# Performance work log

Measured on AMD Instinct MI355X. Metric: run time of the kernel, lower is better.

Reference implementation:

```python
import jax, jax.numpy as jnp
import numpy as np

B, S, H = 2, 1024, 2048          # batch, seq, hidden
E, K = 8, 2                       # num experts, top-k
I = 1408                          # moe_intermediate_size
IS = 5632                         # shared_expert_intermediate_size
WSCALE = 0.02


def setup_inputs() -> dict:
    key = jax.random.key(0)
    ks = jax.random.split(key, 9)
    f32 = jnp.float32
    return {
        "hidden_states": jax.random.normal(ks[0], (B, S, H), dtype=f32),
        "gate_w": jax.random.normal(ks[1], (E, H), dtype=f32) * WSCALE,          # router
        "w_gate": jax.random.normal(ks[2], (E, H, I), dtype=f32) * WSCALE,       # experts.N.gate_proj
        "w_up": jax.random.normal(ks[3], (E, H, I), dtype=f32) * WSCALE,         # experts.N.up_proj
        "w_down": jax.random.normal(ks[4], (E, I, H), dtype=f32) * WSCALE,       # experts.N.down_proj
        "sw_gate": jax.random.normal(ks[5], (H, IS), dtype=f32) * WSCALE,        # shared_expert.gate_proj
        "sw_up": jax.random.normal(ks[6], (H, IS), dtype=f32) * WSCALE,          # shared_expert.up_proj
        "sw_down": jax.random.normal(ks[7], (IS, H), dtype=f32) * WSCALE,        # shared_expert.down_proj
        "shared_gate_w": jax.random.normal(ks[8], (H, 1), dtype=f32) * WSCALE,   # shared_expert_gate
    }


def reference(hidden_states, gate_w, w_gate, w_up, w_down, sw_gate, sw_up, sw_down, shared_gate_w):
    x = hidden_states                                   # [B,S,H]
    # ---- TopKGate: softmax router -> top-k weights + indices, renormalized ----
    logits = jnp.einsum("bsh,eh->bse", x, gate_w)       # [B,S,E]
    probs = jax.nn.softmax(logits, axis=-1)
    top_w, top_i = jax.lax.top_k(probs, K)              # [B,S,K]
    top_w = top_w / jnp.sum(top_w, axis=-1, keepdims=True)
    # dense combine weights per expert: sum_k top_w * (top_i == e)  -> [B,S,E]
    onehot = jax.nn.one_hot(top_i, E, dtype=x.dtype)    # [B,S,K,E]
    combine = jnp.einsum("bsk,bske->bse", top_w, onehot)
    # ---- dense all-experts SwiGLU MLP, then mask/combine (faithful to source) ----
    g = jnp.einsum("bsh,ehi->besi", x, w_gate)          # [B,E,S,I]
    u = jnp.einsum("bsh,ehi->besi", x, w_up)
    h = jax.nn.silu(g) * u
    expert_out = jnp.einsum("besi,eih->besh", h, w_down)  # [B,E,S,H]
    moe_out = jnp.einsum("besh,bse->bsh", expert_out, combine)
    # ---- shared expert with sigmoid gate ----
    sh = jax.nn.silu(x @ sw_gate) * (x @ sw_up)         # [B,S,IS]
    shared_out = sh @ sw_down                            # [B,S,H]
    shared_gate = jax.nn.sigmoid(x @ shared_gate_w)     # [B,S,1]
    return moe_out + shared_out * shared_gate
```

## Files before the change

### kernel.cpp

```cpp
#include <hip/hip_runtime.h>
#include <hip/hip_bf16.h>
#include <stdint.h>

#define TOK   2048
#define HDIM  2048
#define IDIM  1408
#define ISDIM 5632
#define NEXP  8

typedef float  f32x4  __attribute__((ext_vector_type(4)));
typedef short  bf16x8 __attribute__((ext_vector_type(8)));

__device__ __forceinline__ unsigned short f2b(float f) {
  union { float f; uint32_t u; } v; v.f = f;
  return (unsigned short)((v.u + 0x7fffu + ((v.u >> 16) & 1u)) >> 16);
}

__device__ __forceinline__ void async16(void* lds, const void* g) {
  __builtin_amdgcn_global_load_lds(
      (const __attribute__((address_space(1))) unsigned int*)g,
      (__attribute__((address_space(3))) unsigned int*)lds, 16, 0, 0);
}

__global__ __launch_bounds__(256) void router_kernel(
    const float* __restrict__ X, const float* __restrict__ GW,
    const float* __restrict__ SGW, int* __restrict__ cnt,
    int* __restrict__ tok_e, float* __restrict__ tok_w, float* __restrict__ sg)
{
  const int tkn = blockIdx.x, t = threadIdx.x;
  const float* xr = X + (size_t)tkn * HDIM;
  float a[NEXP + 1];
  #pragma unroll
  for (int e = 0; e <= NEXP; ++e) a[e] = 0.f;
  for (int h = t; h < HDIM; h += 256) {
    const float xv = xr[h];
    #pragma unroll
    for (int e = 0; e < NEXP; ++e) a[e] += xv * GW[e * HDIM + h];
    a[NEXP] += xv * SGW[h];
  }
  #pragma unroll
  for (int off = 32; off > 0; off >>= 1) {
    #pragma unroll
    for (int e = 0; e <= NEXP; ++e) a[e] += __shfl_down(a[e], off);
  }
  __shared__ float red[4][NEXP + 1];
  if ((t & 63) == 0) {
    #pragma unroll
    for (int e = 0; e <= NEXP; ++e) red[t >> 6][e] = a[e];
  }
  __syncthreads();
  if (t == 0) {
    float l[NEXP + 1];
    #pragma unroll
    for (int e = 0; e <= NEXP; ++e) l[e] = red[0][e] + red[1][e] + red[2][e] + red[3][e];
    int i1 = 0;
    #pragma unroll
    for (int e = 1; e < NEXP; ++e) if (l[e] > l[i1]) i1 = e;
    int i2 = (i1 == 0) ? 1 : 0;
    #pragma unroll
    for (int e = 0; e < NEXP; ++e) if (e != i1 && e != i2 && l[e] > l[i2]) i2 = e;
    const float w1 = 1.f / (1.f + __expf(l[i2] - l[i1]));
    tok_e[tkn * 2 + 0] = i1; tok_e[tkn * 2 + 1] = i2;
    tok_w[tkn * 2 + 0] = w1; tok_w[tkn * 2 + 1] = 1.f - w1;
    atomicAdd(&cnt[i1], 1); atomicAdd(&cnt[i2], 1);
    sg[tkn] = 1.f / (1.f + __expf(-l[NEXP]));
  }
}

__global__ void scan_kernel(const int* __restrict__ cnt, int* __restrict__ offs) {
  if (threadIdx.x == 0) {
    int r = 0;
    for (int e = 0; e < NEXP; ++e) { offs[e] = r; r += cnt[e]; }
  }
}

__global__ __launch_bounds__(256) void build_kernel(
    const int* __restrict__ tok_e, const float* __restrict__ tok_w,
    const int* __restrict__ offs, int* __restrict__ cur,
    int* __restrict__ list, float* __restrict__ wl)
{
  const int tkn = blockIdx.x * 256 + threadIdx.x;
  if (tkn >= TOK) return;
  #pragma unroll
  for (int k = 0; k < 2; ++k) {
    const int e = tok_e[tkn * 2 + k];
    const int pos = atomicAdd(&cur[e], 1);
    const int slot = offs[e] + pos;
    list[slot] = tkn;
    wl[slot] = tok_w[tkn * 2 + k];
  }
}

__global__ __launch_bounds__(256) void cvt_kernel(
    const float* __restrict__ src, unsigned short* __restrict__ dst, int n4)
{
  const int i = blockIdx.x * 512 + threadIdx.x;
  #pragma unroll
  for (int p = 0; p < 2; ++p) {
    const int j = i + p * 256;
    if (j < n4) {
      const float4 v = ((const float4*)src)[j];
      ushort4 b; b.x = f2b(v.x); b.y = f2b(v.y); b.z = f2b(v.z); b.w = f2b(v.w);
      ((ushort4*)dst)[j] = b;
    }
  }
}

__global__ __launch_bounds__(256) void transpose_cvt_kernel(
    const float* __restrict__ src, unsigned short* __restrict__ dst,
    const int R, const int C)
{
  __shared__ unsigned short tile[64][72];
  const size_t mat = (size_t)blockIdx.z * R * C;
  const int c0 = blockIdx.x * 64, r0 = blockIdx.y * 64;
  const int t = threadIdx.x;
  const int rr = t >> 4, cc = (t & 15) * 4;
  #pragma unroll
  for (int p = 0; p < 4; ++p) {
    const int r = rr + p * 16;
    const float4 v = *(const float4*)(src + mat + (size_t)(r0 + r) * C + c0 + cc);
    tile[cc + 0][r] = f2b(v.x);
    tile[cc + 1][r] = f2b(v.y);
    tile[cc + 2][r] = f2b(v.z);
    tile[cc + 3][r] = f2b(v.w);
  }
  __syncthreads();
  #pragma unroll
  for (int p = 0; p < 2; ++p) {
    const int id = p * 256 + t;
    const int c = id >> 3, q = id & 7;
    const uint4 v = *(const uint4*)&tile[c][q * 8];
    *(uint4*)(dst + mat + (size_t)(c0 + c) * R + r0 + q * 8) = v;
  }
}


template<bool GATHER>
__global__ __launch_bounds__(256) void gateup_bf_kernel(
    const unsigned short* __restrict__ Xb,
    const unsigned short* __restrict__ WgT,
    const unsigned short* __restrict__ WuT,
    unsigned short* __restrict__ Cout,
    const int* __restrict__ list, const int* __restrict__ offs,
    const int* __restrict__ cnt, const int N, const int NT)
{
  __shared__ char smem[49152];
  char* sA  = smem;
  char* sBg = smem + 16384;
  char* sBu = smem + 32768;

  int wg = blockIdx.x;
  wg = (wg & 7) * (gridDim.x >> 3) + (wg >> 3);
  const int mt = wg & 15;
  const int pn = wg >> 4;

  const int t = threadIdx.x;
  int rowbase, mcnt, n0;
  const unsigned short *Wg, *Wu;
  if (GATHER) {
    const int e = pn / NT, n = pn % NT;
    mcnt = cnt[e] - mt * 128;
    if (mcnt <= 0) return;
    rowbase = offs[e] + mt * 128;
    n0 = n * 128;
    Wg = WgT + (size_t)e * N * HDIM;
    Wu = WuT + (size_t)e * N * HDIM;
  } else {
    rowbase = mt * 128;
    mcnt = 128;
    n0 = pn * 128;
    Wg = WgT; Wu = WuT;
  }

  const int w = t >> 6, lane = t & 63;
  const int wr = w >> 1, wc = w & 1;
  const int lcol = lane & 15, lk = lane >> 4;

  f32x4 accg[4][4], accu[4][4];
  #pragma unroll
  for (int i = 0; i < 4; ++i)
    #pragma unroll
    for (int j = 0; j < 4; ++j) { accg[i][j] = {0.f,0.f,0.f,0.f}; accu[i][j] = {0.f,0.f,0.f,0.f}; }

  int arow[4], bm[4], koff[4];
  #pragma unroll
  for (int p = 0; p < 4; ++p) {
    const int s = p * 256 + t;
    const int m = s >> 3;
    bm[p] = m;
    koff[p] = ((s & 7) ^ (m & 7)) << 3;
    arow[p] = GATHER ? list[rowbase + m] : (rowbase + m);
  }

  const int KSTEPS = HDIM / 64;
  for (int kt = 0; kt < KSTEPS; ++kt) {
    const int k0 = kt * 64;
    if (kt) __syncthreads();
    #pragma unroll
    for (int p = 0; p < 4; ++p) {
      const int lb = (p * 256 + (t & 192)) * 16;
      async16(sA  + lb, Xb + (size_t)arow[p] * HDIM + k0 + koff[p]);
      async16(sBg + lb, Wg + (size_t)(n0 + bm[p]) * HDIM + k0 + koff[p]);
      async16(sBu + lb, Wu + (size_t)(n0 + bm[p]) * HDIM + k0 + koff[p]);
    }
    __syncthreads();
    #pragma unroll
    for (int ks = 0; ks < 2; ++ks) {
      bf16x8 af[4], bg[4], bu[4];
      #pragma unroll
      for (int fm = 0; fm < 4; ++fm) {
        const int m = wr * 64 + fm * 16 + lcol;
        af[fm] = *(const bf16x8*)(sA + m * 128 + (((ks * 4 + lk) ^ (m & 7)) << 4));
      }
      #pragma unroll
      for (int fn = 0; fn < 4; ++fn) {
        const int n = wc * 64 + fn * 16 + lcol;
        const int ra = n * 128 + (((ks * 4 + lk) ^ (n & 7)) << 4);
        bg[fn] = *(const bf16x8*)(sBg + ra);
        bu[fn] = *(const bf16x8*)(sBu + ra);
      }
      #pragma unroll
      for (int fm = 0; fm < 4; ++fm)
        #pragma unroll
        for (int fn = 0; fn < 4; ++fn) {
          accg[fm][fn] = __builtin_amdgcn_mfma_f32_16x16x32_bf16(af[fm], bg[fn], accg[fm][fn], 0, 0, 0);
          accu[fm][fn] = __builtin_amdgcn_mfma_f32_16x16x32_bf16(af[fm], bu[fn], accu[fm][fn], 0, 0, 0);
        }
    }
  }
  #pragma unroll
  for (int fm = 0; fm < 4; ++fm) {
    #pragma unroll
    for (int fn = 0; fn < 4; ++fn) {
      const int col = n0 + wc * 64 + fn * 16 + lcol;
      #pragma unroll
      for (int r = 0; r < 4; ++r) {
        const int lrow = wr * 64 + fm * 16 + lk * 4 + r;
        if (lrow < mcnt) {
          const float gv = accg[fm][fn][r];
          const float uv = accu[fm][fn][r];
          const float hv = gv * uv / (1.f + __expf(-gv));
          Cout[(size_t)(rowbase + lrow) * N + col] = f2b(hv);
        }
      }
    }
  }
}

template<bool EXPERT, int KSPLIT>
__global__ __launch_bounds__(256) void down_bf_kernel(
    const unsigned short* __restrict__ Abuf,
    const unsigned short* __restrict__ BT,
    float* __restrict__ out,
    const int* __restrict__ list, const float* __restrict__ wl,
    const int* __restrict__ offs, const int* __restrict__ cnt,
    const int K, const int ktps)
{
  __shared__ char smem[32768];
  char* sA = smem;
  char* sB = smem + 16384;

  int wg = blockIdx.x;
  wg = (wg & 7) * (gridDim.x >> 3) + (wg >> 3);
  const int ksp = wg % KSPLIT;
  const int mt  = (wg / KSPLIT) & 15;
  const int pn  = wg / (KSPLIT * 16);

  const int t = threadIdx.x;
  int rowbase, mcnt, n0;
  const unsigned short* Bm;
  if (EXPERT) {
    const int e = pn >> 4, n = pn & 15;
    mcnt = cnt[e] - mt * 128;
    if (mcnt <= 0) return;
    rowbase = offs[e] + mt * 128;
    n0 = n * 128;
    Bm = BT + (size_t)e * HDIM * K;
  } else {
    rowbase = mt * 128;
    mcnt = 128;
    n0 = pn * 128;
    Bm = BT;
  }
  const int w = t >> 6, lane = t & 63;
  const int wr = w >> 1, wc = w & 1;
  const int lcol = lane & 15, lk = lane >> 4;

  f32x4 acc[4][4];
  #pragma unroll
  for (int i = 0; i < 4; ++i)
    #pragma unroll
    for (int j = 0; j < 4; ++j) acc[i][j] = {0.f,0.f,0.f,0.f};

  int bm[4], koff[4];
  #pragma unroll
  for (int p = 0; p < 4; ++p) {
    const int s = p * 256 + t;
    const int m = s >> 3;
    bm[p] = m;
    koff[p] = ((s & 7) ^ (m & 7)) << 3;
  }

  const int kbeg = ksp * ktps, kend = kbeg + ktps;
  for (int kt = kbeg; kt < kend; ++kt) {
    const int k0 = kt * 64;
    if (kt != kbeg) __syncthreads();
    #pragma unroll
    for (int p = 0; p < 4; ++p) {
      const int lb = (p * 256 + (t & 192)) * 16;
      async16(sA + lb, Abuf + (size_t)(rowbase + bm[p]) * K + k0 + koff[p]);
      async16(sB + lb, Bm + (size_t)(n0 + bm[p]) * K + k0 + koff[p]);
    }
    __syncthreads();
    #pragma unroll
    for (int ks = 0; ks < 2; ++ks) {
      bf16x8 af[4], bfr[4];
      #pragma unroll
      for (int fm = 0; fm < 4; ++fm) {
        const int m = wr * 64 + fm * 16 + lcol;
        af[fm] = *(const bf16x8*)(sA + m * 128 + (((ks * 4 + lk) ^ (m & 7)) << 4));
      }
      #pragma unroll
      for (int fn = 0; fn < 4; ++fn) {
        const int n = wc * 64 + fn * 16 + lcol;
        bfr[fn] = *(const bf16x8*)(sB + n * 128 + (((ks * 4 + lk) ^ (n & 7)) << 4));
      }
      #pragma unroll
      for (int fm = 0; fm < 4; ++fm)
        #pragma unroll
        for (int fn = 0; fn < 4; ++fn)
          acc[fm][fn] = __builtin_amdgcn_mfma_f32_16x16x32_bf16(af[fm], bfr[fn], acc[fm][fn], 0, 0, 0);
    }
  }
  #pragma unroll
  for (int fm = 0; fm < 4; ++fm) {
    #pragma unroll
    for (int fn = 0; fn < 4; ++fn) {
      const int col = n0 + wc * 64 + fn * 16 + lcol;
      #pragma unroll
      for (int r = 0; r < 4; ++r) {
        const int lrow = wr * 64 + fm * 16 + lk * 4 + r;
        if (lrow < mcnt) {
          const float v = acc[fm][fn][r];
          if (EXPERT) {
            const int slot = rowbase + lrow;
            atomicAdd(out + (size_t)list[slot] * HDIM + col, wl[slot] * v);
          } else {
            const int row = rowbase + lrow;
            atomicAdd(out + (size_t)row * HDIM + col, wl[row] * v);
          }
        }
      }
    }
  }
}

template<bool GATHER>
__global__ __launch_bounds__(256) void gateup_kernel(
    const float* __restrict__ X,
    const float* __restrict__ WgA, const float* __restrict__ WuA,
    unsigned short* __restrict__ Cout,
    const int* __restrict__ list, const int* __restrict__ offs,
    const int* __restrict__ cnt, const int N)
{
  __shared__ char smem[49152];
  char* sA  = smem;
  char* sBg = smem + 16384;
  char* sBu = smem + 32768;
  const int t = threadIdx.x;
  const int nt = blockIdx.x;
  int rowbase, mcnt;
  const float *Wg, *Wu;
  if (GATHER) {
    const int e  = blockIdx.y >> 4;
    const int mt = blockIdx.y & 15;
    mcnt = cnt[e] - mt * 128;
    if (mcnt <= 0) return;
    rowbase = offs[e] + mt * 128;
    Wg = WgA + (size_t)e * HDIM * N;
    Wu = WuA + (size_t)e * HDIM * N;
  } else {
    rowbase = blockIdx.y * 128;
    mcnt = 128;
    Wg = WgA; Wu = WuA;
  }
  const int n0 = nt * 128;
  const int w = t >> 6, lane = t & 63;
  const int wr = w >> 1, wc = w & 1;
  const int lcol = lane & 15, lk = lane >> 4;
  f32x4 accg[4][4], accu[4][4];
  #pragma unroll
  for (int i = 0; i < 4; ++i)
    #pragma unroll
    for (int j = 0; j < 4; ++j) { accg[i][j] = {0.f,0.f,0.f,0.f}; accu[i][j] = {0.f,0.f,0.f,0.f}; }
  int arow[8];
  #pragma unroll
  for (int p = 0; p < 8; ++p) {
    const int m = p * 16 + (t >> 4);
    arow[p] = GATHER ? list[rowbase + m] : (rowbase + m);
  }
  const int ak4 = (t & 15) << 2;
  const int bn = t & 127, bkh = t >> 7;
  const int KSTEPS = HDIM / 64;
  for (int kt = 0; kt < KSTEPS; ++kt) {
    const int k0 = kt * 64;
    if (kt) __syncthreads();
    #pragma unroll
    for (int p = 0; p < 8; ++p) {
      const int m = p * 16 + (t >> 4);
      const float4 v = *(const float4*)(X + (size_t)arow[p] * HDIM + k0 + ak4);
      ushort4 b; b.x = f2b(v.x); b.y = f2b(v.y); b.z = f2b(v.z); b.w = f2b(v.w);
      *(ushort4*)(sA + m * 128 + ((((ak4 >> 3) ^ (m & 7)) << 4) | ((ak4 & 7) << 1))) = b;
    }
    #pragma unroll
    for (int p = 0; p < 8; ++p) {
      const int k4 = (p << 1) | bkh;
      const size_t gb = (size_t)(k0 + (k4 << 2)) * N + n0 + bn;
      const int wa = bn * 128 + ((((k4 >> 1) ^ (bn & 7)) << 4) | ((k4 & 1) << 3));
      ushort4 vg, vu;
      vg.x = f2b(Wg[gb]);                 vu.x = f2b(Wu[gb]);
      vg.y = f2b(Wg[gb + (size_t)N]);     vu.y = f2b(Wu[gb + (size_t)N]);
      vg.z = f2b(Wg[gb + 2*(size_t)N]);   vu.z = f2b(Wu[gb + 2*(size_t)N]);
      vg.w = f2b(Wg[gb + 3*(size_t)N]);   vu.w = f2b(Wu[gb + 3*(size_t)N]);
      *(ushort4*)(sBg + wa) = vg;
      *(ushort4*)(sBu + wa) = vu;
    }
    __syncthreads();
    #pragma unroll
    for (int ks = 0; ks < 2; ++ks) {
      bf16x8 af[4], bg[4], bu[4];
      #pragma unroll
      for (int fm = 0; fm < 4; ++fm) {
        const int m = wr * 64 + fm * 16 + lcol;
        af[fm] = *(const bf16x8*)(sA + m * 128 + (((ks * 4 + lk) ^ (m & 7)) << 4));
      }
      #pragma unroll
      for (int fn = 0; fn < 4; ++fn) {
        const int n = wc * 64 + fn * 16 + lcol;
        const int ra = n * 128 + (((ks * 4 + lk) ^ (n & 7)) << 4);
        bg[fn] = *(const bf16x8*)(sBg + ra);
        bu[fn] = *(const bf16x8*)(sBu + ra);
      }
      #pragma unroll
      for (int fm = 0; fm < 4; ++fm)
        #pragma unroll
        for (int fn = 0; fn < 4; ++fn) {
          accg[fm][fn] = __builtin_amdgcn_mfma_f32_16x16x32_bf16(af[fm], bg[fn], accg[fm][fn], 0, 0, 0);
          accu[fm][fn] = __builtin_amdgcn_mfma_f32_16x16x32_bf16(af[fm], bu[fn], accu[fm][fn], 0, 0, 0);
        }
    }
  }
  #pragma unroll
  for (int fm = 0; fm < 4; ++fm) {
    #pragma unroll
    for (int fn = 0; fn < 4; ++fn) {
      const int col = n0 + wc * 64 + fn * 16 + lcol;
      #pragma unroll
      for (int r = 0; r < 4; ++r) {
        const int lrow = wr * 64 + fm * 16 + lk * 4 + r;
        if (lrow < mcnt) {
          const float gv = accg[fm][fn][r];
          const float uv = accu[fm][fn][r];
          Cout[(size_t)(rowbase + lrow) * N + col] = f2b(gv * uv / (1.f + __expf(-gv)));
        }
      }
    }
  }
}

template<bool EXPERT>
__global__ __launch_bounds__(256) void down_kernel(
    const unsigned short* __restrict__ Abuf,
    const float* __restrict__ Ball,
    float* __restrict__ out,
    const int* __restrict__ list, const float* __restrict__ wl,
    const int* __restrict__ offs, const int* __restrict__ cnt, const int K)
{
  __shared__ char smem[32768];
  char* sA = smem;
  char* sB = smem + 16384;
  const int t = threadIdx.x;
  const int nt = blockIdx.x;
  int rowbase, mcnt;
  const float* Bm;
  if (EXPERT) {
    const int e  = blockIdx.y >> 4;
    const int mt = blockIdx.y & 15;
    mcnt = cnt[e] - mt * 128;
    if (mcnt <= 0) return;
    rowbase = offs[e] + mt * 128;
    Bm = Ball + (size_t)e * K * HDIM;
  } else {
    rowbase = blockIdx.y * 128;
    mcnt = 128;
    Bm = Ball;
  }
  const int n0 = nt * 128;
  const int w = t >> 6, lane = t & 63;
  const int wr = w >> 1, wc = w & 1;
  const int lcol = lane & 15, lk = lane >> 4;
  f32x4 acc[4][4];
  #pragma unroll
  for (int i = 0; i < 4; ++i)
    #pragma unroll
    for (int j = 0; j < 4; ++j) acc[i][j] = {0.f,0.f,0.f,0.f};
  const int bn = t & 127, bkh = t >> 7;
  const int KSTEPS = K / 64;
  for (int kt = 0; kt < KSTEPS; ++kt) {
    const int k0 = kt * 64;
    if (kt) __syncthreads();
    #pragma unroll
    for (int p = 0; p < 4; ++p) {
      const int s = p * 256 + t;
      const int m = s >> 3;
      const int k8 = (s & 7) ^ (m & 7);
      const uint4 v = *(const uint4*)(Abuf + (size_t)(rowbase + m) * K + k0 + (k8 << 3));
      *(uint4*)(sA + s * 16) = v;
    }
    #pragma unroll
    for (int p = 0; p < 8; ++p) {
      const int k4 = (p << 1) | bkh;
      const size_t gb = (size_t)(k0 + (k4 << 2)) * HDIM + n0 + bn;
      const int wa = bn * 128 + ((((k4 >> 1) ^ (bn & 7)) << 4) | ((k4 & 1) << 3));
      ushort4 vb;
      vb.x = f2b(Bm[gb]);
      vb.y = f2b(Bm[gb + HDIM]);
      vb.z = f2b(Bm[gb + 2 * HDIM]);
      vb.w = f2b(Bm[gb + 3 * HDIM]);
      *(ushort4*)(sB + wa) = vb;
    }
    __syncthreads();
    #pragma unroll
    for (int ks = 0; ks < 2; ++ks) {
      bf16x8 af[4], bfr[4];
      #pragma unroll
      for (int fm = 0; fm < 4; ++fm) {
        const int m = wr * 64 + fm * 16 + lcol;
        af[fm] = *(const bf16x8*)(sA + m * 128 + (((ks * 4 + lk) ^ (m & 7)) << 4));
      }
      #pragma unroll
      for (int fn = 0; fn < 4; ++fn) {
        const int n = wc * 64 + fn * 16 + lcol;
        bfr[fn] = *(const bf16x8*)(sB + n * 128 + (((ks * 4 + lk) ^ (n & 7)) << 4));
      }
      #pragma unroll
      for (int fm = 0; fm < 4; ++fm)
        #pragma unroll
        for (int fn = 0; fn < 4; ++fn)
          acc[fm][fn] = __builtin_amdgcn_mfma_f32_16x16x32_bf16(af[fm], bfr[fn], acc[fm][fn], 0, 0, 0);
    }
  }
  #pragma unroll
  for (int fm = 0; fm < 4; ++fm) {
    #pragma unroll
    for (int fn = 0; fn < 4; ++fn) {
      const int col = n0 + wc * 64 + fn * 16 + lcol;
      #pragma unroll
      for (int r = 0; r < 4; ++r) {
        const int lrow = wr * 64 + fm * 16 + lk * 4 + r;
        if (lrow < mcnt) {
          const float v = acc[fm][fn][r];
          if (EXPERT) {
            const int slot = rowbase + lrow;
            atomicAdd(out + (size_t)list[slot] * HDIM + col, wl[slot] * v);
          } else {
            const int row = rowbase + lrow;
            out[(size_t)row * HDIM + col] = wl[row] * v;
          }
        }
      }
    }
  }
}

extern "C" void kernel_launch(void* const* d_in, const int* in_sizes, int n_in,
                              void* d_out, int out_size, void* d_ws, size_t ws_size,
                              hipStream_t stream)
{
  const float* x       = (const float*)d_in[0];
  const float* gate_w  = (const float*)d_in[1];
  const float* w_gate  = (const float*)d_in[2];
  const float* w_up    = (const float*)d_in[3];
  const float* w_down  = (const float*)d_in[4];
  const float* sw_gate = (const float*)d_in[5];
  const float* sw_up   = (const float*)d_in[6];
  const float* sw_down = (const float*)d_in[7];
  const float* sgw     = (const float*)d_in[8];

  float* out = (float*)d_out;
  char* ws = (char*)d_ws;

  const size_t NEED = 136000000;

  if (ws_size >= NEED) {
    unsigned short* Xb   = (unsigned short*)ws;
    unsigned short* R1a  = (unsigned short*)(ws + 8388608);
    unsigned short* R1b  = (unsigned short*)(ws + 54525952);
    unsigned short* shb  = (unsigned short*)(ws + 100663296);
    unsigned short* hb   = (unsigned short*)(ws + 123731968);
    char* meta = ws + 135626752;
    int*   cnt   = (int*)(meta);
    int*   cur   = (int*)(meta + 256);
    int*   offs  = (int*)(meta + 512);
    int*   list  = (int*)(meta + 768);
    float* wl    = (float*)(meta + 768 + 17152);
    int*   tok_e = (int*)(meta + 768 + 2 * 17152);
    float* tok_w = (float*)(meta + 768 + 2 * 17152 + 16384);
    float* sg    = (float*)(meta + 768 + 2 * 17152 + 32768);

    hipMemsetAsync(meta, 0, 768 + 2 * 17152, stream);
    hipMemsetAsync(out, 0, (size_t)TOK * HDIM * 4, stream);

    cvt_kernel<<<TOK * HDIM / 4 / 512, 256, 0, stream>>>(x, Xb, TOK * HDIM / 4);
    router_kernel<<<TOK, 256, 0, stream>>>(x, gate_w, sgw, cnt, tok_e, tok_w, sg);
    scan_kernel<<<1, 64, 0, stream>>>(cnt, offs);
    build_kernel<<<8, 256, 0, stream>>>(tok_e, tok_w, offs, cur, list, wl);

    transpose_cvt_kernel<<<dim3(ISDIM / 64, HDIM / 64, 1), 256, 0, stream>>>(sw_gate, R1a, HDIM, ISDIM);
    transpose_cvt_kernel<<<dim3(ISDIM / 64, HDIM / 64, 1), 256, 0, stream>>>(sw_up,   R1b, HDIM, ISDIM);
    gateup_bf_kernel<false><<<704, 256, 0, stream>>>(
        Xb, R1a, R1b, shb, nullptr, nullptr, nullptr, ISDIM, 44);
    transpose_cvt_kernel<<<dim3(HDIM / 64, ISDIM / 64, 1), 256, 0, stream>>>(sw_down, R1a, ISDIM, HDIM);
    down_bf_kernel<false, 2><<<512, 256, 0, stream>>>(
        shb, R1a, out, nullptr, sg, nullptr, nullptr, ISDIM, (ISDIM / 64) / 2);
    transpose_cvt_kernel<<<dim3(IDIM / 64, HDIM / 64, NEXP), 256, 0, stream>>>(w_gate, R1a, HDIM, IDIM);
    transpose_cvt_kernel<<<dim3(IDIM / 64, HDIM / 64, NEXP), 256, 0, stream>>>(w_up,   R1b, HDIM, IDIM);
    gateup_bf_kernel<true><<<1408, 256, 0, stream>>>(
        Xb, R1a, R1b, hb, list, offs, cnt, IDIM, 11);
    transpose_cvt_kernel<<<dim3(HDIM / 64, IDIM / 64, NEXP), 256, 0, stream>>>(w_down, R1a, IDIM, HDIM);
    down_bf_kernel<true, 1><<<2048, 256, 0, stream>>>(
        hb, R1a, out, list, wl, offs, cnt, IDIM, IDIM / 64);
  } else {
    unsigned short* sh_buf = (unsigned short*)ws;
    unsigned short* h_buf  = (unsigned short*)(ws + 23068672);
    char* meta = ws + 34963456;
    int*   cnt   = (int*)(meta);
    int*   cur   = (int*)(meta + 256);
    int*   offs  = (int*)(meta + 512);
    int*   list  = (int*)(meta + 768);
    float* wl    = (float*)(meta + 768 + 17152);
    int*   tok_e = (int*)(meta + 768 + 2 * 17152);
    float* tok_w = (float*)(meta + 768 + 2 * 17152 + 16384);
    float* sg    = (float*)(meta + 768 + 2 * 17152 + 32768);

    hipMemsetAsync(meta, 0, 768 + 2 * 17152, stream);
    router_kernel<<<TOK, 256, 0, stream>>>(x, gate_w, sgw, cnt, tok_e, tok_w, sg);
    scan_kernel<<<1, 64, 0, stream>>>(cnt, offs);
    build_kernel<<<8, 256, 0, stream>>>(tok_e, tok_w, offs, cur, list, wl);
    gateup_kernel<false><<<dim3(ISDIM / 128, TOK / 128), 256, 0, stream>>>(
        x, sw_gate, sw_up, sh_buf, nullptr, nullptr, nullptr, ISDIM);
    down_kernel<false><<<dim3(HDIM / 128, TOK / 128), 256, 0, stream>>>(
        sh_buf, sw_down, out, nullptr, sg, nullptr, nullptr, ISDIM);
    gateup_kernel<true><<<dim3(IDIM / 128, NEXP * 16), 256, 0, stream>>>(
        x, w_gate, w_up, h_buf, list, offs, cnt, IDIM);
    down_kernel<true><<<dim3(HDIM / 128, NEXP * 16), 256, 0, stream>>>(
        h_buf, w_down, out, list, wl, offs, cnt, IDIM);
  }
}
```

Measured before the change: 674.9 us.

## Merge shared and routed expert GEMMs into single gate-up and down launches

Adds a gate-up kernel and a down-projection kernel that each cover both the shared expert and the routed experts in one grid. Block IDs are split by range so that shared and expert tiles run concurrently. This removes the separate launches and the partially filled last waves between the shared and expert phases. It needs a larger workspace so all transposed bf16 weights can be held at once. It also drops the old block-order swizzle and the fp32 fallback path, so a small workspace now leaves no valid code path.

```diff
diff --git a/kernel.cpp b/kernel.cpp
--- a/kernel.cpp
+++ b/kernel.cpp
@@ -134,26 +134,232 @@
   }
 }
 
-
-template<bool GATHER>
-__global__ __launch_bounds__(256) void gateup_bf_kernel(
+__global__ __launch_bounds__(256) void gateup_fused_kernel(
     const unsigned short* __restrict__ Xb,
-    const unsigned short* __restrict__ WgT,
-    const unsigned short* __restrict__ WuT,
-    unsigned short* __restrict__ Cout,
-    const int* __restrict__ list, const int* __restrict__ offs,
-    const int* __restrict__ cnt, const int N, const int NT)
+    const unsigned short* __restrict__ Wshg, const unsigned short* __restrict__ Wshu,
+    const unsigned short* __restrict__ Wexg, const unsigned short* __restrict__ Wexu,
+    unsigned short* __restrict__ shb, unsigned short* __restrict__ hb,
+    const int* __restrict__ list, const int* __restrict__ offs, const int* __restrict__ cnt)
 {
   __shared__ char smem[49152];
   char* sA  = smem;
   char* sBg = smem + 16384;
   char* sBu = smem + 32768;
 
+  const int wg = blockIdx.x;
+  const int mt = wg / 132;
+  const int pn = wg % 132;
+  const int t = threadIdx.x;
+
+  int rowbase, mcnt, n0, N, gather;
+  const unsigned short *Wg, *Wu;
+  unsigned short* Cout;
+  if (pn < 44) {
+    N = ISDIM; n0 = pn * 128; rowbase = mt * 128; mcnt = 128; gather = 0;
+    Wg = Wshg; Wu = Wshu; Cout = shb;
+  } else {
+    const int pnE = pn - 44;
+    const int e = pnE / 11, n = pnE % 11;
+    mcnt = cnt[e] - mt * 128;
+    if (mcnt <= 0) return;
+    N = IDIM; n0 = n * 128; rowbase = offs[e] + mt * 128; gather = 1;
+    Wg = Wexg + (size_t)e * IDIM * HDIM;
+    Wu = Wexu + (size_t)e * IDIM * HDIM;
+    Cout = hb;
+  }
+
+  const int w = t >> 6, lane = t & 63;
+  const int wr = w >> 1, wc = w & 1;
+  const int lcol = lane & 15, lk = lane >> 4;
+
+  f32x4 accg[4][4], accu[4][4];
+  #pragma unroll
+  for (int i = 0; i < 4; ++i)
+    #pragma unroll
+    for (int j = 0; j < 4; ++j) { accg[i][j] = {0.f,0.f,0.f,0.f}; accu[i][j] = {0.f,0.f,0.f,0.f}; }
+
+  int arow[4], bm[4], koff[4];
+  #pragma unroll
+  for (int p = 0; p < 4; ++p) {
+    const int s = p * 256 + t;
+    const int m = s >> 3;
+    bm[p] = m;
+    koff[p] = ((s & 7) ^ (m & 7)) << 3;
+    arow[p] = gather ? list[rowbase + m] : (rowbase + m);
+  }
+
+  const int KSTEPS = HDIM / 64;
+  for (int kt = 0; kt < KSTEPS; ++kt) {
+    const int k0 = kt * 64;
+    if (kt) __syncthreads();
+    #pragma unroll
+    for (int p = 0; p < 4; ++p) {
+      const int lb = (p * 256 + (t & 192)) * 16;
+      async16(sA  + lb, Xb + (size_t)arow[p] * HDIM + k0 + koff[p]);
+      async16(sBg + lb, Wg + (size_t)(n0 + bm[p]) * HDIM + k0 + koff[p]);
+      async16(sBu + lb, Wu + (size_t)(n0 + bm[p]) * HDIM + k0 + koff[p]);
+    }
+    __syncthreads();
+    #pragma unroll
+    for (int ks = 0; ks < 2; ++ks) {
+      bf16x8 af[4], bg[4], bu[4];
+      #pragma unroll
+      for (int fm = 0; fm < 4; ++fm) {
+        const int m = wr * 64 + fm * 16 + lcol;
+        af[fm] = *(const bf16x8*)(sA + m * 128 + (((ks * 4 + lk) ^ (m & 7)) << 4));
+      }
+      #pragma unroll
+      for (int fn = 0; fn < 4; ++fn) {
+        const int n = wc * 64 + fn * 16 + lcol;
+        const int ra = n * 128 + (((ks * 4 + lk) ^ (n & 7)) << 4);
+        bg[fn] = *(const bf16x8*)(sBg + ra);
+        bu[fn] = *(const bf16x8*)(sBu + ra);
+      }
+      #pragma unroll
+      for (int fm = 0; fm < 4; ++fm)
+        #pragma unroll
+        for (int fn = 0; fn < 4; ++fn) {
+          accg[fm][fn] = __builtin_amdgcn_mfma_f32_16x16x32_bf16(af[fm], bg[fn], accg[fm][fn], 0, 0, 0);
+          accu[fm][fn] = __builtin_amdgcn_mfma_f32_16x16x32_bf16(af[fm], bu[fn], accu[fm][fn], 0, 0, 0);
+        }
+    }
+  }
+  #pragma unroll
+  for (int fm = 0; fm < 4; ++fm) {
+    #pragma unroll
+    for (int fn = 0; fn < 4; ++fn) {
+      const int col = n0 + wc * 64 + fn * 16 + lcol;
+      #pragma unroll
+      for (int r = 0; r < 4; ++r) {
+        const int lrow = wr * 64 + fm * 16 + lk * 4 + r;
+        if (lrow < mcnt) {
+          const float gv = accg[fm][fn][r];
+          const float uv = accu[fm][fn][r];
+          const float hv = gv * uv / (1.f + __expf(-gv));
+          Cout[(size_t)(rowbase + lrow) * N + col] = f2b(hv);
+        }
+      }
+    }
+  }
+}
+
+__global__ __launch_bounds__(256) void down_fused_kernel(
+    const unsigned short* __restrict__ shb, const unsigned short* __restrict__ hb,
+    const unsigned short* __restrict__ WdshT, const unsigned short* __restrict__ WdexT,
+    float* __restrict__ out,
+    const int* __restrict__ list, const float* __restrict__ wl, const float* __restrict__ sg,
+    const int* __restrict__ offs, const int* __restrict__ cnt)
+{
+  __shared__ char smem[32768];
+  char* sA = smem;
+  char* sB = smem + 16384;
+
+  const int wg = blockIdx.x;
+  const int t = threadIdx.x;
+  int rowbase, mcnt, n0, K, kbeg, em;
+  const unsigned short *Ap, *Bp;
+  if (wg < 1024) {
+    const int pn = wg & 15, layer = wg >> 4;
+    const int ksp = layer & 3, mt = layer >> 2;
+    rowbase = mt * 128; mcnt = 128; n0 = pn * 128;
+    K = ISDIM; kbeg = ksp * 22; em = 0;
+    Ap = shb; Bp = WdshT;
+  } else {
+    const int wgE = wg - 1024;
+    const int pnE = wgE & 127, mt = wgE >> 7;
+    const int e = pnE >> 4;
+    mcnt = cnt[e] - mt * 128;
+    if (mcnt <= 0) return;
+    rowbase = offs[e] + mt * 128; n0 = (pnE & 15) * 128;
+    K = IDIM; kbeg = 0; em = 1;
+    Ap = hb; Bp = WdexT + (size_t)e * HDIM * IDIM;
+  }
+
+  const int w = t >> 6, lane = t & 63;
+  const int wr = w >> 1, wc = w & 1;
+  const int lcol = lane & 15, lk = lane >> 4;
+
+  f32x4 acc[4][4];
+  #pragma unroll
+  for (int i = 0; i < 4; ++i)
+    #pragma unroll
+    for (int j = 0; j < 4; ++j) acc[i][j] = {0.f,0.f,0.f,0.f};
+
+  int bm[4], koff[4];
+  #pragma unroll
+  for (int p = 0; p < 4; ++p) {
+    const int s = p * 256 + t;
+    const int m = s >> 3;
+    bm[p] = m;
+    koff[p] = ((s & 7) ^ (m & 7)) << 3;
+  }
+
+  for (int kt = kbeg; kt < kbeg + 22; ++kt) {
+    const int k0 = kt * 64;
+    if (kt != kbeg) __syncthreads();
+    #pragma unroll
+    for (int p = 0; p < 4; ++p) {
+      const int lb = (p * 256 + (t & 192)) * 16;
+      async16(sA + lb, Ap + (size_t)(rowbase + bm[p]) * K + k0 + koff[p]);
+      async16(sB + lb, Bp + (size_t)(n0 + bm[p]) * K + k0 + koff[p]);
+    }
+    __syncthreads();
+    #pragma unroll
+    for (int ks = 0; ks < 2; ++ks) {
+      bf16x8 af[4], bfr[4];
+      #pragma unroll
+      for (int fm = 0; fm < 4; ++fm) {
+        const int m = wr * 64 + fm * 16 + lcol;
+        af[fm] = *(const bf16x8*)(sA + m * 128 + (((ks * 4 + lk) ^ (m & 7)) << 4));
+      }
+      #pragma unroll
+      for (int fn = 0; fn < 4; ++fn) {
+        const int n = wc * 64 + fn * 16 + lcol;
+        bfr[fn] = *(const bf16x8*)(sB + n * 128 + (((ks * 4 + lk) ^ (n & 7)) << 4));
+      }
+      #pragma unroll
+      for (int fm = 0; fm < 4; ++fm)
+        #pragma unroll
+        for (int fn = 0; fn < 4; ++fn)
+          acc[fm][fn] = __builtin_amdgcn_mfma_f32_16x16x32_bf16(af[fm], bfr[fn], acc[fm][fn], 0, 0, 0);
+    }
+  }
+  #pragma unroll
+  for (int fm = 0; fm < 4; ++fm) {
+    #pragma unroll
+    for (int fn = 0; fn < 4; ++fn) {
+      const int col = n0 + wc * 64 + fn * 16 + lcol;
+      #pragma unroll
+      for (int r = 0; r < 4; ++r) {
+        const int lrow = wr * 64 + fm * 16 + lk * 4 + r;
+        if (lrow < mcnt) {
+          const float v = acc[fm][fn][r];
+          const int sl = rowbase + lrow;
+          const int orow = em ? list[sl] : sl;
+          const float sc = em ? wl[sl] : sg[sl];
+          atomicAdd(out + (size_t)orow * HDIM + col, sc * v);
+        }
+      }
+    }
+  }
+}
+
+template<bool GATHER>
+__global__ __launch_bounds__(256) void gateup_bf_kernel(
+    const unsigned short* __restrict__ Xb,
+    const unsigned short* __restrict__ WgT, const unsigned short* __restrict__ WuT,
+    unsigned short* __restrict__ Cout,
+    const int* __restrict__ list, const int* __restrict__ offs,
+    const int* __restrict__ cnt, const int N, const int NT)
+{
+  __shared__ char smem[49152];
+  char* sA  = smem;
+  char* sBg = smem + 16384;
+  char* sBu = smem + 32768;
   int wg = blockIdx.x;
   wg = (wg & 7) * (gridDim.x >> 3) + (wg >> 3);
   const int mt = wg & 15;
   const int pn = wg >> 4;
-
   const int t = threadIdx.x;
   int rowbase, mcnt, n0;
   const unsigned short *Wg, *Wu;
@@ -166,22 +372,17 @@
     Wg = WgT + (size_t)e * N * HDIM;
     Wu = WuT + (size_t)e * N * HDIM;
   } else {
-    rowbase = mt * 128;
-    mcnt = 128;
-    n0 = pn * 128;
+    rowbase = mt * 128; mcnt = 128; n0 = pn * 128;
     Wg = WgT; Wu = WuT;
   }
-
   const int w = t >> 6, lane = t & 63;
   const int wr = w >> 1, wc = w & 1;
   const int lcol = lane & 15, lk = lane >> 4;
-
   f32x4 accg[4][4], accu[4][4];
   #pragma unroll
   for (int i = 0; i < 4; ++i)
     #pragma unroll
     for (int j = 0; j < 4; ++j) { accg[i][j] = {0.f,0.f,0.f,0.f}; accu[i][j] = {0.f,0.f,0.f,0.f}; }
-
   int arow[4], bm[4], koff[4];
   #pragma unroll
   for (int p = 0; p < 4; ++p) {
@@ -191,7 +392,6 @@
     koff[p] = ((s & 7) ^ (m & 7)) << 3;
     arow[p] = GATHER ? list[rowbase + m] : (rowbase + m);
   }
-
   const int KSTEPS = HDIM / 64;
   for (int kt = 0; kt < KSTEPS; ++kt) {
     const int k0 = kt * 64;
@@ -239,8 +439,7 @@
         if (lrow < mcnt) {
           const float gv = accg[fm][fn][r];
           const float uv = accu[fm][fn][r];
-          const float hv = gv * uv / (1.f + __expf(-gv));
-          Cout[(size_t)(rowbase + lrow) * N + col] = f2b(hv);
+          Cout[(size_t)(rowbase + lrow) * N + col] = f2b(gv * uv / (1.f + __expf(-gv)));
         }
       }
     }
@@ -259,13 +458,11 @@
   __shared__ char smem[32768];
   char* sA = smem;
   char* sB = smem + 16384;
-
   int wg = blockIdx.x;
   wg = (wg & 7) * (gridDim.x >> 3) + (wg >> 3);
   const int ksp = wg % KSPLIT;
   const int mt  = (wg / KSPLIT) & 15;
   const int pn  = wg / (KSPLIT * 16);
-
   const int t = threadIdx.x;
   int rowbase, mcnt, n0;
   const unsigned short* Bm;
@@ -277,21 +474,17 @@
     n0 = n * 128;
     Bm = BT + (size_t)e * HDIM * K;
   } else {
-    rowbase = mt * 128;
-    mcnt = 128;
-    n0 = pn * 128;
+    rowbase = mt * 128; mcnt = 128; n0 = pn * 128;
     Bm = BT;
   }
   const int w = t >> 6, lane = t & 63;
   const int wr = w >> 1, wc = w & 1;
   const int lcol = lane & 15, lk = lane >> 4;
-
   f32x4 acc[4][4];
   #pragma unroll
   for (int i = 0; i < 4; ++i)
     #pragma unroll
     for (int j = 0; j < 4; ++j) acc[i][j] = {0.f,0.f,0.f,0.f};
-
   int bm[4], koff[4];
   #pragma unroll
   for (int p = 0; p < 4; ++p) {
@@ -300,7 +493,6 @@
     bm[p] = m;
     koff[p] = ((s & 7) ^ (m & 7)) << 3;
   }
-
   const int kbeg = ksp * ktps, kend = kbeg + ktps;
   for (int kt = kbeg; kt < kend; ++kt) {
     const int k0 = kt * 64;
@@ -355,224 +547,6 @@
   }
 }
 
-template<bool GATHER>
-__global__ __launch_bounds__(256) void gateup_kernel(
-    const float* __restrict__ X,
-    const float* __restrict__ WgA, const float* __restrict__ WuA,
-    unsigned short* __restrict__ Cout,
-    const int* __restrict__ list, const int* __restrict__ offs,
-    const int* __restrict__ cnt, const int N)
-{
-  __shared__ char smem[49152];
-  char* sA  = smem;
-  char* sBg = smem + 16384;
-  char* sBu = smem + 32768;
-  const int t = threadIdx.x;
-  const int nt = blockIdx.x;
-  int rowbase, mcnt;
-  const float *Wg, *Wu;
-  if (GATHER) {
-    const int e  = blockIdx.y >> 4;
-    const int mt = blockIdx.y & 15;
-    mcnt = cnt[e] - mt * 128;
-    if (mcnt <= 0) return;
-    rowbase = offs[e] + mt * 128;
-    Wg = WgA + (size_t)e * HDIM * N;
-    Wu = WuA + (size_t)e * HDIM * N;
-  } else {
-    rowbase = blockIdx.y * 128;
-    mcnt = 128;
-    Wg = WgA; Wu = WuA;
-  }
-  const int n0 = nt * 128;
-  const int w = t >> 6, lane = t & 63;
-  const int wr = w >> 1, wc = w & 1;
-  const int lcol = lane & 15, lk = lane >> 4;
-  f32x4 accg[4][4], accu[4][4];
-  #pragma unroll
-  for (int i = 0; i < 4; ++i)
-    #pragma unroll
-    for (int j = 0; j < 4; ++j) { accg[i][j] = {0.f,0.f,0.f,0.f}; accu[i][j] = {0.f,0.f,0.f,0.f}; }
-  int arow[8];
-  #pragma unroll
-  for (int p = 0; p < 8; ++p) {
-    const int m = p * 16 + (t >> 4);
-    arow[p] = GATHER ? list[rowbase + m] : (rowbase + m);
-  }
-  const int ak4 = (t & 15) << 2;
-  const int bn = t & 127, bkh = t >> 7;
-  const int KSTEPS = HDIM / 64;
-  for (int kt = 0; kt < KSTEPS; ++kt) {
-    const int k0 = kt * 64;
-    if (kt) __syncthreads();
-    #pragma unroll
-    for (int p = 0; p < 8; ++p) {
-      const int m = p * 16 + (t >> 4);
-      const float4 v = *(const float4*)(X + (size_t)arow[p] * HDIM + k0 + ak4);
-      ushort4 b; b.x = f2b(v.x); b.y = f2b(v.y); b.z = f2b(v.z); b.w = f2b(v.w);
-      *(ushort4*)(sA + m * 128 + ((((ak4 >> 3) ^ (m & 7)) << 4) | ((ak4 & 7) << 1))) = b;
-    }
-    #pragma unroll
-    for (int p = 0; p < 8; ++p) {
-      const int k4 = (p << 1) | bkh;
-      const size_t gb = (size_t)(k0 + (k4 << 2)) * N + n0 + bn;
-      const int wa = bn * 128 + ((((k4 >> 1) ^ (bn & 7)) << 4) | ((k4 & 1) << 3));
-      ushort4 vg, vu;
-      vg.x = f2b(Wg[gb]);                 vu.x = f2b(Wu[gb]);
-      vg.y = f2b(Wg[gb + (size_t)N]);     vu.y = f2b(Wu[gb + (size_t)N]);
-      vg.z = f2b(Wg[gb + 2*(size_t)N]);   vu.z = f2b(Wu[gb + 2*(size_t)N]);
-      vg.w = f2b(Wg[gb + 3*(size_t)N]);   vu.w = f2b(Wu[gb + 3*(size_t)N]);
-      *(ushort4*)(sBg + wa) = vg;
-      *(ushort4*)(sBu + wa) = vu;
-    }
-    __syncthreads();
-    #pragma unroll
-    for (int ks = 0; ks < 2; ++ks) {
-      bf16x8 af[4], bg[4], bu[4];
-      #pragma unroll
-      for (int fm = 0; fm < 4; ++fm) {
-        const int m = wr * 64 + fm * 16 + lcol;
-        af[fm] = *(const bf16x8*)(sA + m * 128 + (((ks * 4 + lk) ^ (m & 7)) << 4));
-      }
-      #pragma unroll
-      for (int fn = 0; fn < 4; ++fn) {
-        const int n = wc * 64 + fn * 16 + lcol;
-        const int ra = n * 128 + (((ks * 4 + lk) ^ (n & 7)) << 4);
-        bg[fn] = *(const bf16x8*)(sBg + ra);
-        bu[fn] = *(const bf16x8*)(sBu + ra);
-      }
-      #pragma unroll
-      for (int fm = 0; fm < 4; ++fm)
-        #pragma unroll
-        for (int fn = 0; fn < 4; ++fn) {
-          accg[fm][fn] = __builtin_amdgcn_mfma_f32_16x16x32_bf16(af[fm], bg[fn], accg[fm][fn], 0, 0, 0);
-          accu[fm][fn] = __builtin_amdgcn_mfma_f32_16x16x32_bf16(af[fm], bu[fn], accu[fm][fn], 0, 0, 0);
-        }
-    }
-  }
-  #pragma unroll
-  for (int fm = 0; fm < 4; ++fm) {
-    #pragma unroll
-    for (int fn = 0; fn < 4; ++fn) {
-      const int col = n0 + wc * 64 + fn * 16 + lcol;
-      #pragma unroll
-      for (int r = 0; r < 4; ++r) {
-        const int lrow = wr * 64 + fm * 16 + lk * 4 + r;
-        if (lrow < mcnt) {
-          const float gv = accg[fm][fn][r];
-          const float uv = accu[fm][fn][r];
-          Cout[(size_t)(rowbase + lrow) * N + col] = f2b(gv * uv / (1.f + __expf(-gv)));
-        }
-      }
-    }
-  }
-}
-
-template<bool EXPERT>
-__global__ __launch_bounds__(256) void down_kernel(
-    const unsigned short* __restrict__ Abuf,
-    const float* __restrict__ Ball,
-    float* __restrict__ out,
-    const int* __restrict__ list, const float* __restrict__ wl,
-    const int* __restrict__ offs, const int* __restrict__ cnt, const int K)
-{
-  __shared__ char smem[32768];
-  char* sA = smem;
-  char* sB = smem + 16384;
-  const int t = threadIdx.x;
-  const int nt = blockIdx.x;
-  int rowbase, mcnt;
-  const float* Bm;
-  if (EXPERT) {
-    const int e  = blockIdx.y >> 4;
-    const int mt = blockIdx.y & 15;
-    mcnt = cnt[e] - mt * 128;
-    if (mcnt <= 0) return;
-    rowbase = offs[e] + mt * 128;
-    Bm = Ball + (size_t)e * K * HDIM;
-  } else {
-    rowbase = blockIdx.y * 128;
-    mcnt = 128;
-    Bm = Ball;
-  }
-  const int n0 = nt * 128;
-  const int w = t >> 6, lane = t & 63;
-  const int wr = w >> 1, wc = w & 1;
-  const int lcol = lane & 15, lk = lane >> 4;
-  f32x4 acc[4][4];
-  #pragma unroll
-  for (int i = 0; i < 4; ++i)
-    #pragma unroll
-    for (int j = 0; j < 4; ++j) acc[i][j] = {0.f,0.f,0.f,0.f};
-  const int bn = t & 127, bkh = t >> 7;
-  const int KSTEPS = K / 64;
-  for (int kt = 0; kt < KSTEPS; ++kt) {
-    const int k0 = kt * 64;
-    if (kt) __syncthreads();
-    #pragma unroll
-    for (int p = 0; p < 4; ++p) {
-      const int s = p * 256 + t;
-      const int m = s >> 3;
-      const int k8 = (s & 7) ^ (m & 7);
-      const uint4 v = *(const uint4*)(Abuf + (size_t)(rowbase + m) * K + k0 + (k8 << 3));
-      *(uint4*)(sA + s * 16) = v;
-    }
-    #pragma unroll
-    for (int p = 0; p < 8; ++p) {
-      const int k4 = (p << 1) | bkh;
-      const size_t gb = (size_t)(k0 + (k4 << 2)) * HDIM + n0 + bn;
-      const int wa = bn * 128 + ((((k4 >> 1) ^ (bn & 7)) << 4) | ((k4 & 1) << 3));
-      ushort4 vb;
-      vb.x = f2b(Bm[gb]);
-      vb.y = f2b(Bm[gb + HDIM]);
-      vb.z = f2b(Bm[gb + 2 * HDIM]);
-      vb.w = f2b(Bm[gb + 3 * HDIM]);
-      *(ushort4*)(sB + wa) = vb;
-    }
-    __syncthreads();
-    #pragma unroll
-    for (int ks = 0; ks < 2; ++ks) {
-      bf16x8 af[4], bfr[4];
-      #pragma unroll
-      for (int fm = 0; fm < 4; ++fm) {
-        const int m = wr * 64 + fm * 16 + lcol;
-        af[fm] = *(const bf16x8*)(sA + m * 128 + (((ks * 4 + lk) ^ (m & 7)) << 4));
-      }
-      #pragma unroll
-      for (int fn = 0; fn < 4; ++fn) {
-        const int n = wc * 64 + fn * 16 + lcol;
-        bfr[fn] = *(const bf16x8*)(sB + n * 128 + (((ks * 4 + lk) ^ (n & 7)) << 4));
-      }
-      #pragma unroll
-      for (int fm = 0; fm < 4; ++fm)
-        #pragma unroll
-        for (int fn = 0; fn < 4; ++fn)
-          acc[fm][fn] = __builtin_amdgcn_mfma_f32_16x16x32_bf16(af[fm], bfr[fn], acc[fm][fn], 0, 0, 0);
-    }
-  }
-  #pragma unroll
-  for (int fm = 0; fm < 4; ++fm) {
-    #pragma unroll
-    for (int fn = 0; fn < 4; ++fn) {
-      const int col = n0 + wc * 64 + fn * 16 + lcol;
-      #pragma unroll
-      for (int r = 0; r < 4; ++r) {
-        const int lrow = wr * 64 + fm * 16 + lk * 4 + r;
-        if (lrow < mcnt) {
-          const float v = acc[fm][fn][r];
-          if (EXPERT) {
-            const int slot = rowbase + lrow;
-            atomicAdd(out + (size_t)list[slot] * HDIM + col, wl[slot] * v);
-          } else {
-            const int row = rowbase + lrow;
-            out[(size_t)row * HDIM + col] = wl[row] * v;
-          }
-        }
-      }
-    }
-  }
-}
-
 extern "C" void kernel_launch(void* const* d_in, const int* in_sizes, int n_in,
                               void* d_out, int out_size, void* d_ws, size_t ws_size,
                               hipStream_t stream)
@@ -590,9 +564,47 @@
   float* out = (float*)d_out;
   char* ws = (char*)d_ws;
 
-  const size_t NEED = 136000000;
-
-  if (ws_size >= NEED) {
+  const size_t NEED_FUSED = 182000000;
+  const size_t NEED_R4    = 136000000;
+
+  if (ws_size >= NEED_FUSED) {
+    unsigned short* Xb  = (unsigned short*)ws;
+    unsigned short* W1  = (unsigned short*)(ws + 8388608);
+    unsigned short* W2  = (unsigned short*)(ws + 31457280);
+    unsigned short* W3  = (unsigned short*)(ws + 54525952);
+    unsigned short* W4  = (unsigned short*)(ws + 100663296);
+    unsigned short* shb = (unsigned short*)(ws + 146800640);
+    unsigned short* hb  = (unsigned short*)(ws + 169869312);
+    char* meta = ws + 181764096;
+    int*   cnt   = (int*)(meta);
+    int*   cur   = (int*)(meta + 256);
+    int*   offs  = (int*)(meta + 512);
+    int*   list  = (int*)(meta + 768);
+    float* wl    = (float*)(meta + 768 + 17152);
+    int*   tok_e = (int*)(meta + 768 + 2 * 17152);
+    float* tok_w = (float*)(meta + 768 + 2 * 17152 + 16384);
+    float* sg    = (float*)(meta + 768 + 2 * 17152 + 32768);
+
+    hipMemsetAsync(meta, 0, 768 + 2 * 17152, stream);
+    hipMemsetAsync(out, 0, (size_t)TOK * HDIM * 4, stream);
+
+    cvt_kernel<<<TOK * HDIM / 4 / 512, 256, 0, stream>>>(x, Xb, TOK * HDIM / 4);
+    router_kernel<<<TOK, 256, 0, stream>>>(x, gate_w, sgw, cnt, tok_e, tok_w, sg);
+    scan_kernel<<<1, 64, 0, stream>>>(cnt, offs);
+    build_kernel<<<8, 256, 0, stream>>>(tok_e, tok_w, offs, cur, list, wl);
+
+    transpose_cvt_kernel<<<dim3(ISDIM / 64, HDIM / 64, 1), 256, 0, stream>>>(sw_gate, W1, HDIM, ISDIM);
+    transpose_cvt_kernel<<<dim3(ISDIM / 64, HDIM / 64, 1), 256, 0, stream>>>(sw_up,   W2, HDIM, ISDIM);
+    transpose_cvt_kernel<<<dim3(IDIM / 64, HDIM / 64, NEXP), 256, 0, stream>>>(w_gate, W3, HDIM, IDIM);
+    transpose_cvt_kernel<<<dim3(IDIM / 64, HDIM / 64, NEXP), 256, 0, stream>>>(w_up,   W4, HDIM, IDIM);
+
+    gateup_fused_kernel<<<2112, 256, 0, stream>>>(Xb, W1, W2, W3, W4, shb, hb, list, offs, cnt);
+
+    transpose_cvt_kernel<<<dim3(HDIM / 64, ISDIM / 64, 1), 256, 0, stream>>>(sw_down, W1, ISDIM, HDIM);
+    transpose_cvt_kernel<<<dim3(HDIM / 64, IDIM / 64, NEXP), 256, 0, stream>>>(w_down, W3, IDIM, HDIM);
+
+    down_fused_kernel<<<3072, 256, 0, stream>>>(shb, hb, W1, W3, out, list, wl, sg, offs, cnt);
+  } else if (ws_size >= NEED_R4) {
     unsigned short* Xb   = (unsigned short*)ws;
     unsigned short* R1a  = (unsigned short*)(ws + 8388608);
     unsigned short* R1b  = (unsigned short*)(ws + 54525952);
@@ -630,30 +642,5 @@
     transpose_cvt_kernel<<<dim3(HDIM / 64, IDIM / 64, NEXP), 256, 0, stream>>>(w_down, R1a, IDIM, HDIM);
     down_bf_kernel<true, 1><<<2048, 256, 0, stream>>>(
         hb, R1a, out, list, wl, offs, cnt, IDIM, IDIM / 64);
-  } else {
-    unsigned short* sh_buf = (unsigned short*)ws;
-    unsigned short* h_buf  = (unsigned short*)(ws + 23068672);
-    char* meta = ws + 34963456;
-    int*   cnt   = (int*)(meta);
-    int*   cur   = (int*)(meta + 256);
-    int*   offs  = (int*)(meta + 512);
-    int*   list  = (int*)(meta + 768);
-    float* wl    = (float*)(meta + 768 + 17152);
-    int*   tok_e = (int*)(meta + 768 + 2 * 17152);
-    float* tok_w = (float*)(meta + 768 + 2 * 17152 + 16384);
-    float* sg    = (float*)(meta + 768 + 2 * 17152 + 32768);
-
-    hipMemsetAsync(meta, 0, 768 + 2 * 17152, stream);
-    router_kernel<<<TOK, 256, 0, stream>>>(x, gate_w, sgw, cnt, tok_e, tok_w, sg);
-    scan_kernel<<<1, 64, 0, stream>>>(cnt, offs);
-    build_kernel<<<8, 256, 0, stream>>>(tok_e, tok_w, offs, cur, list, wl);
-    gateup_kernel<false><<<dim3(ISDIM / 128, TOK / 128), 256, 0, stream>>>(
-        x, sw_gate, sw_up, sh_buf, nullptr, nullptr, nullptr, ISDIM);
-    down_kernel<false><<<dim3(HDIM / 128, TOK / 128), 256, 0, stream>>>(
-        sh_buf, sw_down, out, nullptr, sg, nullptr, nullptr, ISDIM);
-    gateup_kernel<true><<<dim3(IDIM / 128, NEXP * 16), 256, 0, stream>>>(
-        x, w_gate, w_up, h_buf, list, offs, cnt, IDIM);
-    down_kernel<true><<<dim3(HDIM / 128, NEXP * 16), 256, 0, stream>>>(
-        h_buf, w_down, out, list, wl, offs, cnt, IDIM);
-  }
-}
+  }
+}
```

Result: no change. 667.3 us (-1.1%).
